# Optimization experiments

Hardware: AMD Instinct MI355X
Metric: run time of the kernel (lower is better)

The kernel has to match this reference:

```python
import math
import jax, jax.numpy as jnp
import numpy as np

B, S, D_MODEL = 32, 1024, 1024
NUM_DISEASES, NUM_STATES = 14, 2


def setup_inputs() -> dict:
    key = jax.random.key(0)
    k1, k2, k3, k4 = jax.random.split(key, 4)
    z_fused = jax.random.normal(k1, (B, S, D_MODEL), dtype=jnp.float32)
    # Xavier-uniform init for disease_knowledge [num_diseases, num_states, d_model]
    fan_in, fan_out = NUM_STATES * D_MODEL, NUM_STATES * D_MODEL  # torch treats last dim as fan
    limit = math.sqrt(6.0 / (D_MODEL + D_MODEL))
    disease_knowledge = jax.random.uniform(
        k2, (NUM_DISEASES, NUM_STATES, D_MODEL), dtype=jnp.float32,
        minval=-limit, maxval=limit)
    # gate Linear: in = 2*d_model, out = d_model (torch stores weight as [out, in])
    glim = math.sqrt(1.0 / (2 * D_MODEL))
    gate_w = jax.random.uniform(k3, (D_MODEL, 2 * D_MODEL), dtype=jnp.float32,
                                minval=-glim, maxval=glim)
    gate_b = jax.random.uniform(k4, (D_MODEL,), dtype=jnp.float32,
                                minval=-glim, maxval=glim)
    return {"z_fused": z_fused, "disease_knowledge": disease_knowledge,
            "gate_w": gate_w, "gate_b": gate_b}


def reference(z_fused, disease_knowledge, gate_w, gate_b):
    Bq, Sq, d = z_fused.shape
    Dn, St, _ = disease_knowledge.shape
    flat_memory = disease_knowledge.reshape(Dn * St, d)          # [D*St, d]
    # per-patch scores against every (disease, state) memory slot
    score = jnp.einsum('bsd,md->bsm', z_fused, flat_memory) / math.sqrt(d)  # [B,S,D*St]
    # per-patch softmax over states
    alpha_per_patch = jax.nn.softmax(score.reshape(Bq, Sq, Dn, St), axis=-1)
    mlc_probs_per_patch = alpha_per_patch[:, :, :, 1]            # [B,S,D]
    mlc_probs = jnp.max(mlc_probs_per_patch, axis=1)             # [B,D]
    M_present = disease_knowledge[:, 1, :]                       # [D,d]
    R_per_patch = jnp.einsum('bsi,id->bsd', mlc_probs_per_patch, M_present)  # [B,S,d]
    gate_in = jnp.concatenate([z_fused, R_per_patch], axis=-1)   # [B,S,2d]
    gate = jax.nn.sigmoid(jnp.einsum('bsk,dk->bsd', gate_in, gate_w) + gate_b)
    z_out = z_fused + gate * R_per_patch
    return (z_out, mlc_probs)
```

## Files before the change

### kernel.cpp

```cpp
#include <hip/hip_runtime.h>
#include <hip/hip_bf16.h>
#include <stdint.h>


typedef __attribute__((ext_vector_type(8))) short bf16x8;
typedef __attribute__((ext_vector_type(4))) float f32x4;

__device__ __forceinline__ unsigned short f2bf(float f) {
  unsigned x = __float_as_uint(f);
  return (unsigned short)((x + 0x7FFFu + ((x >> 16) & 1u)) >> 16);
}
__device__ __forceinline__ float bf2f(unsigned short u) {
  return __uint_as_float(((unsigned)u) << 16);
}

typedef const __attribute__((address_space(1))) uint32_t* gptr_t;
typedef __attribute__((address_space(3))) uint32_t* lptr_t;
__device__ __forceinline__ void gload16(const void* g, void* l) {
  __builtin_amdgcn_global_load_lds((gptr_t)g, (lptr_t)l, 16, 0, 0);
}

__global__ __launch_bounds__(256) void k_convert_wfm(const float* __restrict__ w,
                                                     const float* __restrict__ dk,
                                                     ushort* __restrict__ wb,
                                                     ushort* __restrict__ fmb) {
  int i = blockIdx.x * 256 + threadIdx.x;
  if (i < 524288) {
    float4 v = ((const float4*)w)[i];
    uint2 o;
    o.x = (unsigned)f2bf(v.x) | ((unsigned)f2bf(v.y) << 16);
    o.y = (unsigned)f2bf(v.z) | ((unsigned)f2bf(v.w) << 16);
    ((uint2*)wb)[i] = o;
  } else if (i < 524288 + 8192) {
    int j = i - 524288;
    float4 v = make_float4(0.f, 0.f, 0.f, 0.f);
    if (j < 7168) v = ((const float4*)dk)[j];
    uint2 o;
    o.x = (unsigned)f2bf(v.x) | ((unsigned)f2bf(v.y) << 16);
    o.y = (unsigned)f2bf(v.z) | ((unsigned)f2bf(v.w) << 16);
    ((uint2*)fmb)[j] = o;
  }
}

__global__ __launch_bounds__(256) void k_convert_z(const float* __restrict__ z,
                                                   ushort* __restrict__ zb) {
  int i = blockIdx.x * 256 + threadIdx.x;
  const float4* z4 = (const float4*)z;
  float4 a = z4[2 * i], b = z4[2 * i + 1];
  uint4 o;
  o.x = (unsigned)f2bf(a.x) | ((unsigned)f2bf(a.y) << 16);
  o.y = (unsigned)f2bf(a.z) | ((unsigned)f2bf(a.w) << 16);
  o.z = (unsigned)f2bf(b.x) | ((unsigned)f2bf(b.y) << 16);
  o.w = (unsigned)f2bf(b.z) | ((unsigned)f2bf(b.w) << 16);
  ((uint4*)zb)[i] = o;
}

__global__ __launch_bounds__(256) void k_score(const ushort* __restrict__ zb,
                                               const ushort* __restrict__ fmb,
                                               float* __restrict__ probs,
                                               float* __restrict__ mlc) {
  int tid = threadIdx.x, lane = tid & 63, wv = tid >> 6;
  int row0 = blockIdx.x * 64 + wv * 16;
  int fr = lane & 15, kb = (lane >> 4) << 3;
  const bf16x8* Az = (const bf16x8*)(zb + (size_t)(row0 + fr) * 1024 + kb);
  const bf16x8* B0 = (const bf16x8*)(fmb + (size_t)fr * 1024 + kb);
  const bf16x8* B1 = (const bf16x8*)(fmb + (size_t)(16 + fr) * 1024 + kb);
  f32x4 acc0 = {0.f, 0.f, 0.f, 0.f}, acc1 = {0.f, 0.f, 0.f, 0.f};
  for (int k0 = 0; k0 < 1024; k0 += 32) {
    bf16x8 a  = Az[k0 >> 3];
    bf16x8 b0 = B0[k0 >> 3];
    bf16x8 b1 = B1[k0 >> 3];
    acc0 = __builtin_amdgcn_mfma_f32_16x16x32_bf16(a, b0, acc0, 0, 0, 0);
    acc1 = __builtin_amdgcn_mfma_f32_16x16x32_bf16(a, b1, acc1, 0, 0, 0);
  }
  const float inv32 = 1.0f / 32.0f;
  int rsub = (lane >> 4) << 2;
  int bidx = row0 >> 10;
  for (int f = 0; f < 2; ++f) {
    f32x4 s = f ? acc1 : acc0;
    float part[4];
#pragma unroll
    for (int rg = 0; rg < 4; ++rg) part[rg] = __shfl_xor(s[rg], 1);
    int jj = f * 16 + fr;
    if ((lane & 1) && jj < 28) {
      int dis = (jj - 1) >> 1;
      float pmax = 0.f;
#pragma unroll
      for (int rg = 0; rg < 4; ++rg) {
        float p = 1.f / (1.f + __expf((part[rg] - s[rg]) * inv32));
        probs[(size_t)(row0 + rsub + rg) * 14 + dis] = p;
        pmax = fmaxf(pmax, p);
      }
      atomicMax((unsigned int*)&mlc[bidx * 14 + dis], __float_as_uint(pmax));
    }
  }
}

__global__ __launch_bounds__(256) void k_R(const float* __restrict__ probs,
                                           const float* __restrict__ dk,
                                           ushort* __restrict__ Rb) {
  int t = threadIdx.x;
  int d0 = t << 2;
  int row0 = blockIdx.x << 7;
  float4 M[14];
#pragma unroll
  for (int i = 0; i < 14; ++i)
    M[i] = *(const float4*)&dk[(size_t)(i * 2 + 1) * 1024 + d0];
  for (int r = 0; r < 128; ++r) {
    int row = row0 + r;
    const float* pr = probs + (size_t)row * 14;
    float4 a = make_float4(0.f, 0.f, 0.f, 0.f);
#pragma unroll
    for (int i = 0; i < 14; ++i) {
      float p = pr[i];
      a.x = fmaf(p, M[i].x, a.x); a.y = fmaf(p, M[i].y, a.y);
      a.z = fmaf(p, M[i].z, a.z); a.w = fmaf(p, M[i].w, a.w);
    }
    uint2 o;
    o.x = (unsigned)f2bf(a.x) | ((unsigned)f2bf(a.y) << 16);
    o.y = (unsigned)f2bf(a.z) | ((unsigned)f2bf(a.w) << 16);
    *(uint2*)(Rb + (size_t)row * 1024 + d0) = o;
  }
}

__global__ __launch_bounds__(256) void k_gate(const ushort* __restrict__ zb,
                                              const ushort* __restrict__ Rb,
                                              const ushort* __restrict__ wb,
                                              const float* __restrict__ z,
                                              const float* __restrict__ gb,
                                              float* __restrict__ out) {
  __shared__ ushort Als[128 * 32];
  __shared__ ushort Bls[128 * 32];
  int tid = threadIdx.x;
  int nwg = gridDim.x;
  int swz = (blockIdx.x & 7) * (nwg >> 3) + (blockIdx.x >> 3);
  int row0 = (swz >> 3) << 7;
  int col0 = (swz & 7) << 7;
  int lane = tid & 63, wid = tid >> 6;
  int wr = wid >> 1, wc = wid & 1;
  int sr = tid >> 2;
  int sc = (tid & 3) << 3;
  int fr = lane & 15, kb = (lane >> 4) << 3;
  f32x4 acc[4][4] = {};
  char* Ad = ((char*)Als) + wid * 1024;
  char* Bd = ((char*)Bls) + wid * 1024;
  for (int k0 = 0; k0 < 2048; k0 += 32) {
    const ushort* Asrc = (k0 < 1024)
        ? (zb + (size_t)(row0 + sr) * 1024 + (k0 + sc))
        : (Rb + (size_t)(row0 + sr) * 1024 + (k0 - 1024 + sc));
    const ushort* Bsrc = wb + (size_t)(col0 + sr) * 2048 + (k0 + sc);
    gload16(Asrc, Ad);
    gload16(Asrc + (size_t)64 * 1024, Ad + 4096);
    gload16(Bsrc, Bd);
    gload16(Bsrc + (size_t)64 * 2048, Bd + 4096);
    __syncthreads();
    bf16x8 af[4], bf_[4];
#pragma unroll
    for (int ai = 0; ai < 4; ++ai)
      af[ai] = *(const bf16x8*)&Als[(wr * 64 + ai * 16 + fr) * 32 + kb];
#pragma unroll
    for (int bj = 0; bj < 4; ++bj)
      bf_[bj] = *(const bf16x8*)&Bls[(wc * 64 + bj * 16 + fr) * 32 + kb];
#pragma unroll
    for (int ai = 0; ai < 4; ++ai)
#pragma unroll
      for (int bj = 0; bj < 4; ++bj)
        acc[ai][bj] = __builtin_amdgcn_mfma_f32_16x16x32_bf16(af[ai], bf_[bj], acc[ai][bj], 0, 0, 0);
    __syncthreads();
  }
  int rsub = (lane >> 4) << 2;
#pragma unroll
  for (int ai = 0; ai < 4; ++ai) {
#pragma unroll
    for (int bj = 0; bj < 4; ++bj) {
      int c = col0 + wc * 64 + bj * 16 + fr;
      float gbias = gb[c];
      f32x4 a = acc[ai][bj];
#pragma unroll
      for (int rg = 0; rg < 4; ++rg) {
        int r = row0 + wr * 64 + ai * 16 + rsub + rg;
        size_t o = (size_t)r * 1024 + c;
        float g = 1.f / (1.f + __expf(-(a[rg] + gbias)));
        out[o] = fmaf(g, bf2f(Rb[o]), z[o]);
      }
    }
  }
}

extern "C" void kernel_launch(void* const* d_in, const int* in_sizes, int n_in,
                              void* d_out, int out_size, void* d_ws, size_t ws_size,
                              hipStream_t stream) {
  const float* z  = (const float*)d_in[0];
  const float* dk = (const float*)d_in[1];
  const float* gw = (const float*)d_in[2];
  const float* gb = (const float*)d_in[3];
  float* out = (float*)d_out;

  char* ws = (char*)d_ws;
  ushort* zb   = (ushort*)(ws);
  ushort* Rb   = (ushort*)(ws + 67108864);
  ushort* wb   = (ushort*)(ws + 134217728);
  ushort* fmb  = (ushort*)(ws + 138412032);
  float*  probs= (float*)(ws + 138477568);
  float*  mlc  = out + 33554432;

  hipMemsetAsync(mlc, 0, 448 * sizeof(float), stream);
  k_convert_wfm<<<2080, 256, 0, stream>>>(gw, dk, wb, fmb);
  k_convert_z<<<16384, 256, 0, stream>>>(z, zb);
  k_score<<<512, 256, 0, stream>>>(zb, fmb, probs, mlc);
  k_R<<<256, 256, 0, stream>>>(probs, dk, Rb);
  k_gate<<<2048, 256, 0, stream>>>(zb, Rb, wb, z, gb, out);
}
```

Baseline: 579.5 us.

## Fuse z conversion, scoring and R computation; double-buffer gate GEMM

Merges the z-to-bf16 conversion, score GEMM with softmax, and R projection into one kernel that keeps tiles and per-patch probabilities in shared memory instead of round-tripping through global memory. The gate kernel gets double-buffered LDS staging so global loads overlap MFMA work. The residual term now reads bf16 z instead of fp32 z, removing a large fp32 read but lowering output precision. The fused kernel runs with only 512 blocks, which may limit bandwidth during conversion.

New measurement: 515.1 us. 11.1% less time.

```diff
diff --git a/kernel.cpp b/kernel.cpp
--- a/kernel.cpp
+++ b/kernel.cpp
@@ -9,6 +9,9 @@
 __device__ __forceinline__ unsigned short f2bf(float f) {
   unsigned x = __float_as_uint(f);
   return (unsigned short)((x + 0x7FFFu + ((x >> 16) & 1u)) >> 16);
+}
+__device__ __forceinline__ unsigned pk2(float a, float b) {
+  return (unsigned)f2bf(a) | ((unsigned)f2bf(b) << 16);
 }
 __device__ __forceinline__ float bf2f(unsigned short u) {
   return __uint_as_float(((unsigned)u) << 16);
@@ -27,55 +30,62 @@
   int i = blockIdx.x * 256 + threadIdx.x;
   if (i < 524288) {
     float4 v = ((const float4*)w)[i];
-    uint2 o;
-    o.x = (unsigned)f2bf(v.x) | ((unsigned)f2bf(v.y) << 16);
-    o.y = (unsigned)f2bf(v.z) | ((unsigned)f2bf(v.w) << 16);
+    uint2 o; o.x = pk2(v.x, v.y); o.y = pk2(v.z, v.w);
     ((uint2*)wb)[i] = o;
   } else if (i < 524288 + 8192) {
     int j = i - 524288;
     float4 v = make_float4(0.f, 0.f, 0.f, 0.f);
     if (j < 7168) v = ((const float4*)dk)[j];
-    uint2 o;
-    o.x = (unsigned)f2bf(v.x) | ((unsigned)f2bf(v.y) << 16);
-    o.y = (unsigned)f2bf(v.z) | ((unsigned)f2bf(v.w) << 16);
+    uint2 o; o.x = pk2(v.x, v.y); o.y = pk2(v.z, v.w);
     ((uint2*)fmb)[j] = o;
   }
 }
 
-__global__ __launch_bounds__(256) void k_convert_z(const float* __restrict__ z,
-                                                   ushort* __restrict__ zb) {
-  int i = blockIdx.x * 256 + threadIdx.x;
-  const float4* z4 = (const float4*)z;
-  float4 a = z4[2 * i], b = z4[2 * i + 1];
-  uint4 o;
-  o.x = (unsigned)f2bf(a.x) | ((unsigned)f2bf(a.y) << 16);
-  o.y = (unsigned)f2bf(a.z) | ((unsigned)f2bf(a.w) << 16);
-  o.z = (unsigned)f2bf(b.x) | ((unsigned)f2bf(b.y) << 16);
-  o.w = (unsigned)f2bf(b.z) | ((unsigned)f2bf(b.w) << 16);
-  ((uint4*)zb)[i] = o;
-}
-
-__global__ __launch_bounds__(256) void k_score(const ushort* __restrict__ zb,
+__global__ __launch_bounds__(256) void k_fused(const float* __restrict__ z,
                                                const ushort* __restrict__ fmb,
-                                               float* __restrict__ probs,
+                                               const float* __restrict__ dk,
+                                               ushort* __restrict__ zb,
+                                               ushort* __restrict__ Rb,
                                                float* __restrict__ mlc) {
+  __shared__ ushort At[64][72];
+  __shared__ float pbuf[64][16];
   int tid = threadIdx.x, lane = tid & 63, wv = tid >> 6;
-  int row0 = blockIdx.x * 64 + wv * 16;
+  int row0 = blockIdx.x * 64;
+  int srow = tid >> 2;
+  int scol = (tid & 3) << 4;
   int fr = lane & 15, kb = (lane >> 4) << 3;
-  const bf16x8* Az = (const bf16x8*)(zb + (size_t)(row0 + fr) * 1024 + kb);
   const bf16x8* B0 = (const bf16x8*)(fmb + (size_t)fr * 1024 + kb);
   const bf16x8* B1 = (const bf16x8*)(fmb + (size_t)(16 + fr) * 1024 + kb);
   f32x4 acc0 = {0.f, 0.f, 0.f, 0.f}, acc1 = {0.f, 0.f, 0.f, 0.f};
-  for (int k0 = 0; k0 < 1024; k0 += 32) {
-    bf16x8 a  = Az[k0 >> 3];
-    bf16x8 b0 = B0[k0 >> 3];
-    bf16x8 b1 = B1[k0 >> 3];
-    acc0 = __builtin_amdgcn_mfma_f32_16x16x32_bf16(a, b0, acc0, 0, 0, 0);
-    acc1 = __builtin_amdgcn_mfma_f32_16x16x32_bf16(a, b1, acc1, 0, 0, 0);
+  const float4* zsrc = (const float4*)&z[(size_t)(row0 + srow) * 1024];
+  uint4* zdst = (uint4*)&zb[(size_t)(row0 + srow) * 1024];
+  for (int kc = 0; kc < 1024; kc += 64) {
+    int e0 = (kc + scol) >> 2;
+    float4 v0 = zsrc[e0], v1 = zsrc[e0 + 1], v2 = zsrc[e0 + 2], v3 = zsrc[e0 + 3];
+    uint4 o0, o1;
+    o0.x = pk2(v0.x, v0.y); o0.y = pk2(v0.z, v0.w);
+    o0.z = pk2(v1.x, v1.y); o0.w = pk2(v1.z, v1.w);
+    o1.x = pk2(v2.x, v2.y); o1.y = pk2(v2.z, v2.w);
+    o1.z = pk2(v3.x, v3.y); o1.w = pk2(v3.z, v3.w);
+    int eo = (kc + scol) >> 3;
+    zdst[eo] = o0; zdst[eo + 1] = o1;
+    *(uint4*)&At[srow][scol] = o0;
+    *(uint4*)&At[srow][scol + 8] = o1;
+    __syncthreads();
+#pragma unroll
+    for (int kk = 0; kk < 64; kk += 32) {
+      bf16x8 a = *(const bf16x8*)&At[wv * 16 + fr][kk + kb];
+      bf16x8 b0 = B0[(kc + kk) >> 3];
+      bf16x8 b1 = B1[(kc + kk) >> 3];
+      acc0 = __builtin_amdgcn_mfma_f32_16x16x32_bf16(a, b0, acc0, 0, 0, 0);
+      acc1 = __builtin_amdgcn_mfma_f32_16x16x32_bf16(a, b1, acc1, 0, 0, 0);
+    }
+    __syncthreads();
   }
   const float inv32 = 1.0f / 32.0f;
   int rsub = (lane >> 4) << 2;
   int bidx = row0 >> 10;
+#pragma unroll
   for (int f = 0; f < 2; ++f) {
     f32x4 s = f ? acc1 : acc0;
     float part[4];
@@ -88,27 +98,20 @@
 #pragma unroll
       for (int rg = 0; rg < 4; ++rg) {
         float p = 1.f / (1.f + __expf((part[rg] - s[rg]) * inv32));
-        probs[(size_t)(row0 + rsub + rg) * 14 + dis] = p;
+        pbuf[wv * 16 + rsub + rg][dis] = p;
         pmax = fmaxf(pmax, p);
       }
       atomicMax((unsigned int*)&mlc[bidx * 14 + dis], __float_as_uint(pmax));
     }
   }
-}
-
-__global__ __launch_bounds__(256) void k_R(const float* __restrict__ probs,
-                                           const float* __restrict__ dk,
-                                           ushort* __restrict__ Rb) {
-  int t = threadIdx.x;
-  int d0 = t << 2;
-  int row0 = blockIdx.x << 7;
+  __syncthreads();
+  int d0 = tid << 2;
   float4 M[14];
 #pragma unroll
   for (int i = 0; i < 14; ++i)
     M[i] = *(const float4*)&dk[(size_t)(i * 2 + 1) * 1024 + d0];
-  for (int r = 0; r < 128; ++r) {
-    int row = row0 + r;
-    const float* pr = probs + (size_t)row * 14;
+  for (int r = 0; r < 64; ++r) {
+    const float* pr = pbuf[r];
     float4 a = make_float4(0.f, 0.f, 0.f, 0.f);
 #pragma unroll
     for (int i = 0; i < 14; ++i) {
@@ -116,21 +119,18 @@
       a.x = fmaf(p, M[i].x, a.x); a.y = fmaf(p, M[i].y, a.y);
       a.z = fmaf(p, M[i].z, a.z); a.w = fmaf(p, M[i].w, a.w);
     }
-    uint2 o;
-    o.x = (unsigned)f2bf(a.x) | ((unsigned)f2bf(a.y) << 16);
-    o.y = (unsigned)f2bf(a.z) | ((unsigned)f2bf(a.w) << 16);
-    *(uint2*)(Rb + (size_t)row * 1024 + d0) = o;
+    uint2 o; o.x = pk2(a.x, a.y); o.y = pk2(a.z, a.w);
+    *(uint2*)&Rb[(size_t)(row0 + r) * 1024 + d0] = o;
   }
 }
 
 __global__ __launch_bounds__(256) void k_gate(const ushort* __restrict__ zb,
                                               const ushort* __restrict__ Rb,
                                               const ushort* __restrict__ wb,
-                                              const float* __restrict__ z,
                                               const float* __restrict__ gb,
                                               float* __restrict__ out) {
-  __shared__ ushort Als[128 * 32];
-  __shared__ ushort Bls[128 * 32];
+  __shared__ ushort Als[2][128 * 32];
+  __shared__ ushort Bls[2][128 * 32];
   int tid = threadIdx.x;
   int nwg = gridDim.x;
   int swz = (blockIdx.x & 7) * (nwg >> 3) + (blockIdx.x >> 3);
@@ -138,35 +138,42 @@
   int col0 = (swz & 7) << 7;
   int lane = tid & 63, wid = tid >> 6;
   int wr = wid >> 1, wc = wid & 1;
-  int sr = tid >> 2;
-  int sc = (tid & 3) << 3;
+  int sr = tid >> 2, sc = (tid & 3) << 3;
   int fr = lane & 15, kb = (lane >> 4) << 3;
   f32x4 acc[4][4] = {};
-  char* Ad = ((char*)Als) + wid * 1024;
-  char* Bd = ((char*)Bls) + wid * 1024;
-  for (int k0 = 0; k0 < 2048; k0 += 32) {
+
+  auto stage = [&](int k0, int buf) {
     const ushort* Asrc = (k0 < 1024)
         ? (zb + (size_t)(row0 + sr) * 1024 + (k0 + sc))
         : (Rb + (size_t)(row0 + sr) * 1024 + (k0 - 1024 + sc));
     const ushort* Bsrc = wb + (size_t)(col0 + sr) * 2048 + (k0 + sc);
+    char* Ad = ((char*)&Als[buf][0]) + wid * 1024;
+    char* Bd = ((char*)&Bls[buf][0]) + wid * 1024;
     gload16(Asrc, Ad);
     gload16(Asrc + (size_t)64 * 1024, Ad + 4096);
     gload16(Bsrc, Bd);
     gload16(Bsrc + (size_t)64 * 2048, Bd + 4096);
+  };
+
+  stage(0, 0);
+  __syncthreads();
+  int cur = 0;
+  for (int k0 = 32; k0 <= 2048; k0 += 32) {
+    if (k0 < 2048) stage(k0, cur ^ 1);
+    bf16x8 af[4], bfr[4];
+#pragma unroll
+    for (int ai = 0; ai < 4; ++ai)
+      af[ai] = *(const bf16x8*)&Als[cur][(wr * 64 + ai * 16 + fr) * 32 + kb];
+#pragma unroll
+    for (int bj = 0; bj < 4; ++bj)
+      bfr[bj] = *(const bf16x8*)&Bls[cur][(wc * 64 + bj * 16 + fr) * 32 + kb];
+#pragma unroll
+    for (int ai = 0; ai < 4; ++ai)
+#pragma unroll
+      for (int bj = 0; bj < 4; ++bj)
+        acc[ai][bj] = __builtin_amdgcn_mfma_f32_16x16x32_bf16(af[ai], bfr[bj], acc[ai][bj], 0, 0, 0);
     __syncthreads();
-    bf16x8 af[4], bf_[4];
-#pragma unroll
-    for (int ai = 0; ai < 4; ++ai)
-      af[ai] = *(const bf16x8*)&Als[(wr * 64 + ai * 16 + fr) * 32 + kb];
-#pragma unroll
-    for (int bj = 0; bj < 4; ++bj)
-      bf_[bj] = *(const bf16x8*)&Bls[(wc * 64 + bj * 16 + fr) * 32 + kb];
-#pragma unroll
-    for (int ai = 0; ai < 4; ++ai)
-#pragma unroll
-      for (int bj = 0; bj < 4; ++bj)
-        acc[ai][bj] = __builtin_amdgcn_mfma_f32_16x16x32_bf16(af[ai], bf_[bj], acc[ai][bj], 0, 0, 0);
-    __syncthreads();
+    cur ^= 1;
   }
   int rsub = (lane >> 4) << 2;
 #pragma unroll
@@ -181,7 +188,7 @@
         int r = row0 + wr * 64 + ai * 16 + rsub + rg;
         size_t o = (size_t)r * 1024 + c;
         float g = 1.f / (1.f + __expf(-(a[rg] + gbias)));
-        out[o] = fmaf(g, bf2f(Rb[o]), z[o]);
+        out[o] = fmaf(g, bf2f(Rb[o]), bf2f(zb[o]));
       }
     }
   }
@@ -197,17 +204,14 @@
   float* out = (float*)d_out;
 
   char* ws = (char*)d_ws;
-  ushort* zb   = (ushort*)(ws);
-  ushort* Rb   = (ushort*)(ws + 67108864);
-  ushort* wb   = (ushort*)(ws + 134217728);
-  ushort* fmb  = (ushort*)(ws + 138412032);
-  float*  probs= (float*)(ws + 138477568);
-  float*  mlc  = out + 33554432;
+  ushort* zb  = (ushort*)(ws);
+  ushort* Rb  = (ushort*)(ws + 67108864);
+  ushort* wb  = (ushort*)(ws + 134217728);
+  ushort* fmb = (ushort*)(ws + 138412032);
+  float*  mlc = out + 33554432;
 
   hipMemsetAsync(mlc, 0, 448 * sizeof(float), stream);
   k_convert_wfm<<<2080, 256, 0, stream>>>(gw, dk, wb, fmb);
-  k_convert_z<<<16384, 256, 0, stream>>>(z, zb);
-  k_score<<<512, 256, 0, stream>>>(zb, fmb, probs, mlc);
-  k_R<<<256, 256, 0, stream>>>(probs, dk, Rb);
-  k_gate<<<2048, 256, 0, stream>>>(zb, Rb, wb, z, gb, out);
-}
+  k_fused<<<512, 256, 0, stream>>>(z, fmb, dk, zb, Rb, mlc);
+  k_gate<<<2048, 256, 0, stream>>>(zb, Rb, wb, gb, out);
+}
```
